# Performance work log

Measured on AMD Instinct MI355X. Metric: run time of the kernel, lower is better.

Reference implementation:

```python
import jax, jax.numpy as jnp
import numpy as np

N_GROUPS = 1024   # n
L = 128           # keys per group
R = 4             # queries per group (nq[i] == R)
NQ_TOTAL = N_GROUPS * R
D_Q = 256
D_K = 256
D_Z = 256
D_V = 256


def setup_inputs() -> dict:
    key = jax.random.key(0)
    ks = jax.random.split(key, 8)
    nq = jnp.full((N_GROUPS,), R, dtype=jnp.int32)
    q = jax.random.normal(ks[0], (NQ_TOTAL, D_Q), dtype=jnp.float32)
    k = jax.random.normal(ks[1], (N_GROUPS, L, D_K), dtype=jnp.float32)
    v = jax.random.normal(ks[2], (N_GROUPS, L, D_V), dtype=jnp.float32)
    m = jax.random.uniform(ks[3], (N_GROUPS, L)) < 0.9
    m = m.at[:, 0].set(True)  # guarantee each row has at least one valid key
    Wq = jax.random.normal(ks[4], (D_Q, D_Z), dtype=jnp.float32) / np.sqrt(D_Q)
    bq = jnp.zeros((D_Z,), dtype=jnp.float32)
    Wk = jax.random.normal(ks[5], (D_K, D_Z), dtype=jnp.float32) / np.sqrt(D_K)
    bk = jnp.zeros((D_Z,), dtype=jnp.float32)
    return {"nq": nq, "q": q, "k": k, "v": v, "m": m,
            "Wq": Wq, "bq": bq, "Wk": Wk, "bk": bk}


def reference(nq, q, v, k, m, Wq, bq, Wk, bk):
    # Linear projections (nn.Linear with bias)
    qz = q @ Wq + bq                      # (N, d_z)
    kz = k @ Wk + bk                      # (n, l, d_z)
    d_z = Wq.shape[1]
    n = m.shape[0]
    # group index per query: equivalent to repeat_interleave(nq, 0)
    gidx = jnp.repeat(jnp.arange(n), nq, total_repeat_length=q.shape[0])  # (N,)
    # scores: s[i, l] = <kz[group(i), l], qz[i]> / sqrt(d_z)
    s = jnp.einsum('ild,id->il', kz[gidx], qz) / jnp.sqrt(jnp.asarray(d_z, qz.dtype))
    s = jnp.where(m[gidx], s, -jnp.inf)   # masked_fill(~m, -inf)
    p = jax.nn.softmax(s, axis=-1)        # softmax over key dim l
    # weighted sum over keys: (N, d)
    return jnp.einsum('il,ild->id', p, v[gidx])
```

## Files before the change

### kernel.cpp

```cpp
#include <hip/hip_runtime.h>

#define D 256
#define LKEYS 128
#define NGROUP 1024
#define NQ 4096

#define MMAT_OFF 0
#define RVEC_OFF (D * D)
#define U_OFF    (RVEC_OFF + D)
#define WS_FLOATS (U_OFF + NQ * D)

#define DOT4(a, b) ((a).x*(b).x + (a).y*(b).y + (a).z*(b).z + (a).w*(b).w)

__global__ __launch_bounds__(256) void prep_kernel(
    const float* __restrict__ Wq, const float* __restrict__ Wk,
    const float* __restrict__ bq, float* __restrict__ Mmat,
    float* __restrict__ rvec)
{
    __shared__ float wq_s[32][65];
    __shared__ float wk_s[32][65];
    __shared__ float bq_s[64];
    const int t  = threadIdx.x;
    const int a0 = (int)(blockIdx.x >> 3) * 32;
    const int b0 = (int)(blockIdx.x & 7) * 32;
    const int ai = t >> 4;
    const int bj = t & 15;
    float acc00 = 0.f, acc01 = 0.f, acc10 = 0.f, acc11 = 0.f;
    float racc = 0.f;
    for (int z0 = 0; z0 < D; z0 += 64) {
        __syncthreads();
        #pragma unroll
        for (int i = 0; i < 2; ++i) {
            const int f4i = t + 256 * i;
            const int row = f4i >> 4;
            const int c   = (f4i & 15) * 4;
            float4 aa = *(const float4*)&Wq[(size_t)(a0 + row) * D + z0 + c];
            wq_s[row][c] = aa.x; wq_s[row][c+1] = aa.y; wq_s[row][c+2] = aa.z; wq_s[row][c+3] = aa.w;
            float4 bb = *(const float4*)&Wk[(size_t)(b0 + row) * D + z0 + c];
            wk_s[row][c] = bb.x; wk_s[row][c+1] = bb.y; wk_s[row][c+2] = bb.z; wk_s[row][c+3] = bb.w;
        }
        if (t < 64) bq_s[t] = bq[z0 + t];
        __syncthreads();
        #pragma unroll 8
        for (int z = 0; z < 64; ++z) {
            const float wq0 = wq_s[ai][z];
            const float wq1 = wq_s[ai + 16][z];
            const float wk0 = wk_s[bj][z];
            const float wk1 = wk_s[bj + 16][z];
            acc00 += wq0 * wk0; acc01 += wq0 * wk1;
            acc10 += wq1 * wk0; acc11 += wq1 * wk1;
        }
        if (a0 == 0 && t < 32) {
            #pragma unroll 8
            for (int z = 0; z < 64; ++z) racc += bq_s[z] * wk_s[t][z];
        }
    }
    Mmat[(size_t)(a0 + ai)      * D + b0 + bj]      = acc00;
    Mmat[(size_t)(a0 + ai)      * D + b0 + bj + 16] = acc01;
    Mmat[(size_t)(a0 + ai + 16) * D + b0 + bj]      = acc10;
    Mmat[(size_t)(a0 + ai + 16) * D + b0 + bj + 16] = acc11;
    if (a0 == 0 && t < 32) rvec[b0 + t] = racc;
}

__global__ __launch_bounds__(256) void u_gemm_kernel(
    const float* __restrict__ q, const float* __restrict__ Mmat,
    const float* __restrict__ rvec, float* __restrict__ uout)
{
    __shared__ float q_s[16][D];
    const int b = blockIdx.x, t = threadIdx.x, lane = t & 63, w = t >> 6;
    {
        const float4* qg = (const float4*)(q + (size_t)b * 16 * D);
        float4* qs4 = (float4*)q_s;
        #pragma unroll
        for (int i = 0; i < 4; ++i) qs4[t + 256 * i] = qg[t + 256 * i];
    }
    __syncthreads();

    const float4* M4 = (const float4*)Mmat;
    const int r0 = w * 4;
    float4 a0 = {0,0,0,0}, a1 = {0,0,0,0}, a2 = {0,0,0,0}, a3 = {0,0,0,0};
    #pragma unroll 4
    for (int kk = 0; kk < D; ++kk) {
        const float4 m4 = M4[kk * 64 + lane];
        const float qa = q_s[r0 + 0][kk], qb = q_s[r0 + 1][kk];
        const float qc = q_s[r0 + 2][kk], qd = q_s[r0 + 3][kk];
        a0.x += qa*m4.x; a0.y += qa*m4.y; a0.z += qa*m4.z; a0.w += qa*m4.w;
        a1.x += qb*m4.x; a1.y += qb*m4.y; a1.z += qb*m4.z; a1.w += qb*m4.w;
        a2.x += qc*m4.x; a2.y += qc*m4.y; a2.z += qc*m4.z; a2.w += qc*m4.w;
        a3.x += qd*m4.x; a3.y += qd*m4.y; a3.z += qd*m4.z; a3.w += qd*m4.w;
    }
    const float4 r4 = ((const float4*)rvec)[lane];
    float4* U4 = (float4*)uout;
    float4 o;
    o.x=(a0.x+r4.x)*0.0625f; o.y=(a0.y+r4.y)*0.0625f; o.z=(a0.z+r4.z)*0.0625f; o.w=(a0.w+r4.w)*0.0625f;
    U4[((size_t)b * 16 + r0 + 0) * 64 + lane] = o;
    o.x=(a1.x+r4.x)*0.0625f; o.y=(a1.y+r4.y)*0.0625f; o.z=(a1.z+r4.z)*0.0625f; o.w=(a1.w+r4.w)*0.0625f;
    U4[((size_t)b * 16 + r0 + 1) * 64 + lane] = o;
    o.x=(a2.x+r4.x)*0.0625f; o.y=(a2.y+r4.y)*0.0625f; o.z=(a2.z+r4.z)*0.0625f; o.w=(a2.w+r4.w)*0.0625f;
    U4[((size_t)b * 16 + r0 + 2) * 64 + lane] = o;
    o.x=(a3.x+r4.x)*0.0625f; o.y=(a3.y+r4.y)*0.0625f; o.z=(a3.z+r4.z)*0.0625f; o.w=(a3.w+r4.w)*0.0625f;
    U4[((size_t)b * 16 + r0 + 3) * 64 + lane] = o;
}

__global__ __launch_bounds__(256, 4) void attn4_kernel(
    const float* __restrict__ k, const float* __restrict__ v,
    const int* __restrict__ m, const float* __restrict__ uws,
    float* __restrict__ out)
{
    const int g = blockIdx.x, t = threadIdx.x, lane = t & 63, w = t >> 6;

    __shared__ float4 part_s[4][4][64];
    __shared__ float  p_t[LKEYS][4];

    const float4* U4 = (const float4*)(uws + (size_t)g * 4 * D);
    const float4 u0 = U4[0 * 64 + lane];
    const float4 u1 = U4[1 * 64 + lane];
    const float4 u2 = U4[2 * 64 + lane];
    const float4 u3 = U4[3 * 64 + lane];

    const int mk = (lane < 32) ? m[(size_t)g * LKEYS + w * 32 + lane] : 0;
    const unsigned long long bal = __ballot(mk != 0);

    const float4* kg = (const float4*)(k + ((size_t)g * LKEYS + w * 32) * D);
    const float4* vg = (const float4*)(v + ((size_t)g * LKEYS + w * 32) * D);

    #pragma unroll
    for (int it = 0; it < 8; ++it) {
        const int kb = it * 4;
        const float4 ka0 = kg[(kb + 0) * 64 + lane];
        const float4 ka1 = kg[(kb + 1) * 64 + lane];
        const float4 ka2 = kg[(kb + 2) * 64 + lane];
        const float4 ka3 = kg[(kb + 3) * 64 + lane];

        float v16[16];
        v16[ 0]=DOT4(ka0,u0); v16[ 1]=DOT4(ka0,u1); v16[ 2]=DOT4(ka0,u2); v16[ 3]=DOT4(ka0,u3);
        v16[ 4]=DOT4(ka1,u0); v16[ 5]=DOT4(ka1,u1); v16[ 6]=DOT4(ka1,u2); v16[ 7]=DOT4(ka1,u3);
        v16[ 8]=DOT4(ka2,u0); v16[ 9]=DOT4(ka2,u1); v16[10]=DOT4(ka2,u2); v16[11]=DOT4(ka2,u3);
        v16[12]=DOT4(ka3,u0); v16[13]=DOT4(ka3,u1); v16[14]=DOT4(ka3,u2); v16[15]=DOT4(ka3,u3);

        float v8[8];
        { const int hb = lane & 1;
          #pragma unroll
          for (int i = 0; i < 8; ++i) {
              const float keep = hb ? v16[8 + i] : v16[i];
              const float send = hb ? v16[i]     : v16[8 + i];
              v8[i] = keep + __shfl_xor(send, 1);
          } }
        float v4a[4];
        { const int hb = (lane >> 1) & 1;
          #pragma unroll
          for (int i = 0; i < 4; ++i) {
              const float keep = hb ? v8[4 + i] : v8[i];
              const float send = hb ? v8[i]     : v8[4 + i];
              v4a[i] = keep + __shfl_xor(send, 2);
          } }
        float v2a[2];
        { const int hb = (lane >> 2) & 1;
          #pragma unroll
          for (int i = 0; i < 2; ++i) {
              const float keep = hb ? v4a[2 + i] : v4a[i];
              const float send = hb ? v4a[i]     : v4a[2 + i];
              v2a[i] = keep + __shfl_xor(send, 4);
          } }
        float v1;
        { const int hb = (lane >> 3) & 1;
          const float keep = hb ? v2a[1] : v2a[0];
          const float send = hb ? v2a[0] : v2a[1];
          v1 = keep + __shfl_xor(send, 8); }
        v1 += __shfl_xor(v1, 16);
        v1 += __shfl_xor(v1, 32);

        if (lane < 16) {
            const int i  = ((lane & 1) << 3) | ((lane & 2) << 1) | ((lane & 4) >> 1) | ((lane & 8) >> 3);
            const int kl = kb + (i >> 2);
            p_t[w * 32 + kl][i & 3] = ((bal >> kl) & 1ull) ? v1 : -1e30f;
        }
    }
    __syncthreads();

    {
        const float s0 = p_t[lane][w];
        const float s1 = p_t[lane + 64][w];
        float mx = fmaxf(s0, s1);
        #pragma unroll
        for (int off = 32; off > 0; off >>= 1) mx = fmaxf(mx, __shfl_xor(mx, off));
        const float e0 = __expf(s0 - mx);
        const float e1 = __expf(s1 - mx);
        float su = e0 + e1;
        #pragma unroll
        for (int off = 32; off > 0; off >>= 1) su += __shfl_xor(su, off);
        const float inv = 1.0f / su;
        p_t[lane][w]      = e0 * inv;
        p_t[lane + 64][w] = e1 * inv;
    }
    __syncthreads();

    float4 a0 = {0,0,0,0}, a1 = {0,0,0,0}, a2 = {0,0,0,0}, a3 = {0,0,0,0};
    #pragma unroll
    for (int it = 0; it < 4; ++it) {
        const int base = it * 8;
        float4 va[8];
        #pragma unroll
        for (int j = 0; j < 8; ++j) va[j] = vg[(base + j) * 64 + lane];
        #pragma unroll
        for (int j = 0; j < 8; ++j) {
            const float4 pr = *(const float4*)&p_t[w * 32 + base + j][0];
            const float4 vv = va[j];
            a0.x += pr.x*vv.x; a0.y += pr.x*vv.y; a0.z += pr.x*vv.z; a0.w += pr.x*vv.w;
            a1.x += pr.y*vv.x; a1.y += pr.y*vv.y; a1.z += pr.y*vv.z; a1.w += pr.y*vv.w;
            a2.x += pr.z*vv.x; a2.y += pr.z*vv.y; a2.z += pr.z*vv.z; a2.w += pr.z*vv.w;
            a3.x += pr.w*vv.x; a3.y += pr.w*vv.y; a3.z += pr.w*vv.z; a3.w += pr.w*vv.w;
        }
    }

    part_s[w][0][lane] = a0; part_s[w][1][lane] = a1;
    part_s[w][2][lane] = a2; part_s[w][3][lane] = a3;
    __syncthreads();
    {
        const float4 r0 = part_s[0][w][lane];
        const float4 r1 = part_s[1][w][lane];
        const float4 r2 = part_s[2][w][lane];
        const float4 r3 = part_s[3][w][lane];
        float4 o;
        o.x = r0.x + r1.x + r2.x + r3.x;
        o.y = r0.y + r1.y + r2.y + r3.y;
        o.z = r0.z + r1.z + r2.z + r3.z;
        o.w = r0.w + r1.w + r2.w + r3.w;
        ((float4*)(out + ((size_t)g * 4 + w) * D))[lane] = o;
    }
}

__global__ __launch_bounds__(256) void attn_kernel(
    const float* __restrict__ q, const float* __restrict__ k,
    const float* __restrict__ v, const int* __restrict__ m,
    const float* __restrict__ Mmat, const float* __restrict__ rvec,
    float* __restrict__ out)
{
    const int g    = blockIdx.x;
    const int t    = threadIdx.x;
    const int lane = t & 63;
    const int w    = t >> 6;

    __shared__ float  q_s[4][D];
    __shared__ float4 part_s[4][4][64];
    __shared__ float4 u_s4[4][64];
    __shared__ float  p_s[4][LKEYS];
    __shared__ int    m_s[LKEYS];

    {
        const float4* qg = (const float4*)(q + (size_t)g * 4 * D);
        ((float4*)q_s)[t] = qg[t];
    }
    if (t < LKEYS) m_s[t] = m[(size_t)g * LKEYS + t];
    __syncthreads();
    {
        const float4* M4 = (const float4*)Mmat;
        float4 p0 = {0,0,0,0}, p1 = {0,0,0,0}, p2 = {0,0,0,0}, p3 = {0,0,0,0};
        const int base = w * 64;
        #pragma unroll 4
        for (int dd = 0; dd < 64; ++dd) {
            const int a = base + dd;
            const float4 m4 = M4[a * 64 + lane];
            const float q0 = q_s[0][a], q1 = q_s[1][a], q2 = q_s[2][a], q3 = q_s[3][a];
            p0.x += q0*m4.x; p0.y += q0*m4.y; p0.z += q0*m4.z; p0.w += q0*m4.w;
            p1.x += q1*m4.x; p1.y += q1*m4.y; p1.z += q1*m4.z; p1.w += q1*m4.w;
            p2.x += q2*m4.x; p2.y += q2*m4.y; p2.z += q2*m4.z; p2.w += q2*m4.w;
            p3.x += q3*m4.x; p3.y += q3*m4.y; p3.z += q3*m4.z; p3.w += q3*m4.w;
        }
        part_s[w][0][lane] = p0; part_s[w][1][lane] = p1;
        part_s[w][2][lane] = p2; part_s[w][3][lane] = p3;
    }
    __syncthreads();
    {
        float4 acc = ((const float4*)rvec)[lane];
        const float4 a0 = part_s[0][w][lane], a1 = part_s[1][w][lane];
        const float4 a2 = part_s[2][w][lane], a3 = part_s[3][w][lane];
        acc.x += a0.x + a1.x + a2.x + a3.x;
        acc.y += a0.y + a1.y + a2.y + a3.y;
        acc.z += a0.z + a1.z + a2.z + a3.z;
        acc.w += a0.w + a1.w + a2.w + a3.w;
        u_s4[w][lane] = acc;
    }
    __syncthreads();

    const float4 u0 = u_s4[0][lane], u1 = u_s4[1][lane];
    const float4 u2 = u_s4[2][lane], u3 = u_s4[3][lane];
    {
        const float4* kg = (const float4*)(k + (size_t)g * LKEYS * D);
        auto reduce_qt = [&](float d0, float d1, float d2, float d3) -> float {
            float keepA = (lane & 1) ? d1 : d0;
            float sendA = (lane & 1) ? d0 : d1;
            keepA += __shfl_xor(sendA, 1);
            float keepB = (lane & 1) ? d3 : d2;
            float sendB = (lane & 1) ? d2 : d3;
            keepB += __shfl_xor(sendB, 1);
            float keep = (lane & 2) ? keepB : keepA;
            float send = (lane & 2) ? keepA : keepB;
            keep += __shfl_xor(send, 2);
            keep += __shfl_xor(keep, 4);
            keep += __shfl_xor(keep, 8);
            keep += __shfl_xor(keep, 16);
            keep += __shfl_xor(keep, 32);
            return keep;
        };
        const int l0 = w * 32;
        for (int kk = 0; kk < 32; kk += 4) {
            const int l = l0 + kk;
            const float4 kA = kg[(l + 0) * 64 + lane];
            const float4 kB = kg[(l + 1) * 64 + lane];
            const float4 kC = kg[(l + 2) * 64 + lane];
            const float4 kD = kg[(l + 3) * 64 + lane];
            float dA0 = DOT4(kA,u0), dA1 = DOT4(kA,u1), dA2 = DOT4(kA,u2), dA3 = DOT4(kA,u3);
            float dB0 = DOT4(kB,u0), dB1 = DOT4(kB,u1), dB2 = DOT4(kB,u2), dB3 = DOT4(kB,u3);
            float dC0 = DOT4(kC,u0), dC1 = DOT4(kC,u1), dC2 = DOT4(kC,u2), dC3 = DOT4(kC,u3);
            float dD0 = DOT4(kD,u0), dD1 = DOT4(kD,u1), dD2 = DOT4(kD,u2), dD3 = DOT4(kD,u3);
            const float rA = reduce_qt(dA0, dA1, dA2, dA3);
            const float rB = reduce_qt(dB0, dB1, dB2, dB3);
            const float rC = reduce_qt(dC0, dC1, dC2, dC3);
            const float rD = reduce_qt(dD0, dD1, dD2, dD3);
            if (lane < 4) {
                p_s[lane][l + 0] = m_s[l + 0] ? rA * 0.0625f : -1e30f;
                p_s[lane][l + 1] = m_s[l + 1] ? rB * 0.0625f : -1e30f;
                p_s[lane][l + 2] = m_s[l + 2] ? rC * 0.0625f : -1e30f;
                p_s[lane][l + 3] = m_s[l + 3] ? rD * 0.0625f : -1e30f;
            }
        }
    }
    __syncthreads();
    {
        const float v0 = p_s[w][lane];
        const float v1 = p_s[w][lane + 64];
        float mx = fmaxf(v0, v1);
        #pragma unroll
        for (int off = 32; off > 0; off >>= 1) mx = fmaxf(mx, __shfl_xor(mx, off));
        const float e0 = __expf(v0 - mx);
        const float e1 = __expf(v1 - mx);
        float sm = e0 + e1;
        #pragma unroll
        for (int off = 32; off > 0; off >>= 1) sm += __shfl_xor(sm, off);
        const float inv = 1.0f / sm;
        p_s[w][lane]      = e0 * inv;
        p_s[w][lane + 64] = e1 * inv;
    }
    {
        const float4* vg = (const float4*)(v + (size_t)g * LKEYS * D);
        float4 acc = {0,0,0,0};
        #pragma unroll 8
        for (int l = 0; l < LKEYS; ++l) {
            const float pw = p_s[w][l];
            const float4 vv = vg[l * 64 + lane];
            acc.x += pw * vv.x; acc.y += pw * vv.y;
            acc.z += pw * vv.z; acc.w += pw * vv.w;
        }
        float4* og = (float4*)(out + ((size_t)g * 4 + w) * D);
        og[lane] = acc;
    }
}

extern "C" void kernel_launch(void* const* d_in, const int* in_sizes, int n_in,
                              void* d_out, int out_size, void* d_ws, size_t ws_size,
                              hipStream_t stream) {
    const float* q  = (const float*)d_in[1];
    const float* k  = (const float*)d_in[2];
    const float* v  = (const float*)d_in[3];
    const int*   m  = (const int*)  d_in[4];
    const float* Wq = (const float*)d_in[5];
    const float* bq = (const float*)d_in[6];
    const float* Wk = (const float*)d_in[7];

    float* ws = (float*)d_ws;
    prep_kernel<<<64, 256, 0, stream>>>(Wq, Wk, bq, ws + MMAT_OFF, ws + RVEC_OFF);

    if (ws_size >= (size_t)WS_FLOATS * sizeof(float)) {
        u_gemm_kernel<<<NQ / 16, 256, 0, stream>>>(q, ws + MMAT_OFF, ws + RVEC_OFF, ws + U_OFF);
        attn4_kernel<<<NGROUP, 256, 0, stream>>>(k, v, m, ws + U_OFF, (float*)d_out);
    } else {
        attn_kernel<<<NGROUP, 256, 0, stream>>>(q, k, v, m, ws + MMAT_OFF, ws + RVEC_OFF,
                                                (float*)d_out);
    }
}
```

Measured before the change: 83.70 us.

## Split each group's keys across two blocks with flash-style softmax combine

The attention kernel now splits each group's 128 keys into two halves, each handled by its own block (2048 blocks). Each block writes unnormalized partial outputs plus its local max and sum to workspace. A new combine kernel merges the two halves with rescaling. The aim is more parallelism and occupancy for the memory-bound key/value streaming. The cost is an extra launch, extra workspace traffic, and a larger workspace requirement, which could send execution to the fallback path if the workspace is too small.

```diff
diff --git a/kernel.cpp b/kernel.cpp
--- a/kernel.cpp
+++ b/kernel.cpp
@@ -8,7 +8,9 @@
 #define MMAT_OFF 0
 #define RVEC_OFF (D * D)
 #define U_OFF    (RVEC_OFF + D)
-#define WS_FLOATS (U_OFF + NQ * D)
+#define PART_OFF (U_OFF + NQ * D)
+#define PART_STRIDE 260
+#define WS_FLOATS (PART_OFF + 2 * NQ * PART_STRIDE)
 
 #define DOT4(a, b) ((a).x*(b).x + (a).y*(b).y + (a).z*(b).z + (a).w*(b).w)
 
@@ -102,15 +104,17 @@
     U4[((size_t)b * 16 + r0 + 3) * 64 + lane] = o;
 }
 
-__global__ __launch_bounds__(256, 4) void attn4_kernel(
+__global__ __launch_bounds__(256, 8) void attn5_kernel(
     const float* __restrict__ k, const float* __restrict__ v,
     const int* __restrict__ m, const float* __restrict__ uws,
-    float* __restrict__ out)
+    float* __restrict__ part)
 {
-    const int g = blockIdx.x, t = threadIdx.x, lane = t & 63, w = t >> 6;
+    const int b = blockIdx.x;
+    const int g = b >> 1, h = b & 1;
+    const int t = threadIdx.x, lane = t & 63, w = t >> 6;
 
     __shared__ float4 part_s[4][4][64];
-    __shared__ float  p_t[LKEYS][4];
+    __shared__ float  p_t[64][4];
 
     const float4* U4 = (const float4*)(uws + (size_t)g * 4 * D);
     const float4 u0 = U4[0 * 64 + lane];
@@ -118,15 +122,16 @@
     const float4 u2 = U4[2 * 64 + lane];
     const float4 u3 = U4[3 * 64 + lane];
 
-    const int mk = (lane < 32) ? m[(size_t)g * LKEYS + w * 32 + lane] : 0;
+    const int kofs = h * 64;
+    const int mk = m[(size_t)g * LKEYS + kofs + lane];
     const unsigned long long bal = __ballot(mk != 0);
 
-    const float4* kg = (const float4*)(k + ((size_t)g * LKEYS + w * 32) * D);
-    const float4* vg = (const float4*)(v + ((size_t)g * LKEYS + w * 32) * D);
+    const float4* kg = (const float4*)(k + ((size_t)g * LKEYS + kofs) * D);
+    const float4* vg = (const float4*)(v + ((size_t)g * LKEYS + kofs) * D);
 
     #pragma unroll
-    for (int it = 0; it < 8; ++it) {
-        const int kb = it * 4;
+    for (int it = 0; it < 4; ++it) {
+        const int kb = w * 16 + it * 4;
         const float4 ka0 = kg[(kb + 0) * 64 + lane];
         const float4 ka1 = kg[(kb + 1) * 64 + lane];
         const float4 ka2 = kg[(kb + 2) * 64 + lane];
@@ -173,38 +178,37 @@
         if (lane < 16) {
             const int i  = ((lane & 1) << 3) | ((lane & 2) << 1) | ((lane & 4) >> 1) | ((lane & 8) >> 3);
             const int kl = kb + (i >> 2);
-            p_t[w * 32 + kl][i & 3] = ((bal >> kl) & 1ull) ? v1 : -1e30f;
-        }
-    }
-    __syncthreads();
-
-    {
-        const float s0 = p_t[lane][w];
-        const float s1 = p_t[lane + 64][w];
-        float mx = fmaxf(s0, s1);
+            p_t[kl][i & 3] = ((bal >> kl) & 1ull) ? v1 : -1e30f;
+        }
+    }
+    __syncthreads();
+
+    float m_loc, su;
+    {
+        const float s = p_t[lane][w];
+        float mx = s;
         #pragma unroll
         for (int off = 32; off > 0; off >>= 1) mx = fmaxf(mx, __shfl_xor(mx, off));
-        const float e0 = __expf(s0 - mx);
-        const float e1 = __expf(s1 - mx);
-        float su = e0 + e1;
-        #pragma unroll
-        for (int off = 32; off > 0; off >>= 1) su += __shfl_xor(su, off);
-        const float inv = 1.0f / su;
-        p_t[lane][w]      = e0 * inv;
-        p_t[lane + 64][w] = e1 * inv;
+        const bool valid = (bal >> lane) & 1ull;
+        const float e = valid ? __expf(s - mx) : 0.f;
+        float ss = e;
+        #pragma unroll
+        for (int off = 32; off > 0; off >>= 1) ss += __shfl_xor(ss, off);
+        p_t[lane][w] = e;
+        m_loc = mx; su = ss;
     }
     __syncthreads();
 
     float4 a0 = {0,0,0,0}, a1 = {0,0,0,0}, a2 = {0,0,0,0}, a3 = {0,0,0,0};
     #pragma unroll
-    for (int it = 0; it < 4; ++it) {
-        const int base = it * 8;
+    for (int it = 0; it < 2; ++it) {
+        const int base = w * 16 + it * 8;
         float4 va[8];
         #pragma unroll
         for (int j = 0; j < 8; ++j) va[j] = vg[(base + j) * 64 + lane];
         #pragma unroll
         for (int j = 0; j < 8; ++j) {
-            const float4 pr = *(const float4*)&p_t[w * 32 + base + j][0];
+            const float4 pr = *(const float4*)&p_t[base + j][0];
             const float4 vv = va[j];
             a0.x += pr.x*vv.x; a0.y += pr.x*vv.y; a0.z += pr.x*vv.z; a0.w += pr.x*vv.w;
             a1.x += pr.y*vv.x; a1.y += pr.y*vv.y; a1.z += pr.y*vv.z; a1.w += pr.y*vv.w;
@@ -226,8 +230,33 @@
         o.y = r0.y + r1.y + r2.y + r3.y;
         o.z = r0.z + r1.z + r2.z + r3.z;
         o.w = r0.w + r1.w + r2.w + r3.w;
-        ((float4*)(out + ((size_t)g * 4 + w) * D))[lane] = o;
-    }
+        float* pb = part + ((size_t)h * NQ + (size_t)g * 4 + w) * PART_STRIDE;
+        ((float4*)pb)[lane] = o;
+        if (lane == 0) { pb[256] = m_loc; pb[257] = su; }
+    }
+}
+
+__global__ __launch_bounds__(256) void combine_kernel(
+    const float* __restrict__ part, float* __restrict__ out)
+{
+    const int b = blockIdx.x, t = threadIdx.x, lane = t & 63, w = t >> 6;
+    const int i = b * 4 + w;
+    const float* pA = part + (size_t)i * PART_STRIDE;
+    const float* pB = part + ((size_t)NQ + i) * PART_STRIDE;
+    const float mA = pA[256], suA = pA[257];
+    const float mB = pB[256], suB = pB[257];
+    const float Mx = fmaxf(mA, mB);
+    const float fA = __expf(mA - Mx);
+    const float fB = __expf(mB - Mx);
+    const float inv = 1.0f / (fA * suA + fB * suB);
+    const float4 aA = ((const float4*)pA)[lane];
+    const float4 aB = ((const float4*)pB)[lane];
+    float4 o;
+    o.x = (fA*aA.x + fB*aB.x) * inv;
+    o.y = (fA*aA.y + fB*aB.y) * inv;
+    o.z = (fA*aA.z + fB*aB.z) * inv;
+    o.w = (fA*aA.w + fB*aB.w) * inv;
+    ((float4*)out)[(size_t)i * 64 + lane] = o;
 }
 
 __global__ __launch_bounds__(256) void attn_kernel(
@@ -373,7 +402,8 @@
 
     if (ws_size >= (size_t)WS_FLOATS * sizeof(float)) {
         u_gemm_kernel<<<NQ / 16, 256, 0, stream>>>(q, ws + MMAT_OFF, ws + RVEC_OFF, ws + U_OFF);
-        attn4_kernel<<<NGROUP, 256, 0, stream>>>(k, v, m, ws + U_OFF, (float*)d_out);
+        attn5_kernel<<<NGROUP * 2, 256, 0, stream>>>(k, v, m, ws + U_OFF, ws + PART_OFF);
+        combine_kernel<<<NGROUP, 256, 0, stream>>>(ws + PART_OFF, (float*)d_out);
     } else {
         attn_kernel<<<NGROUP, 256, 0, stream>>>(q, k, v, m, ws + MMAT_OFF, ws + RVEC_OFF,
                                                 (float*)d_out);
```

New measurement: 104.0 us. 24.3% more time.

## Fuse query-projection GEMM into attention kernel, drop separate u_gemm launch

Applied to the files above, without the earlier changes.

Each attention block now projects its own four queries through Mmat (loading q into shared memory, partial sums per wave, shared-memory reduction) before the score/softmax/value stages, instead of calling a separate u_gemm kernel that wrote U to workspace. This removes one kernel launch and the write and reread of the 4 MB U buffer. In exchange every block streams the full 256 KB Mmat (mostly served from cache), adds two extra block barriers, and drops the occupancy hint of 4 blocks per unit from launch_bounds.

```diff
diff --git a/kernel.cpp b/kernel.cpp
--- a/kernel.cpp
+++ b/kernel.cpp
@@ -3,12 +3,10 @@
 #define D 256
 #define LKEYS 128
 #define NGROUP 1024
-#define NQ 4096
 
 #define MMAT_OFF 0
 #define RVEC_OFF (D * D)
-#define U_OFF    (RVEC_OFF + D)
-#define WS_FLOATS (U_OFF + NQ * D)
+#define WS_FLOATS (RVEC_OFF + D)
 
 #define DOT4(a, b) ((a).x*(b).x + (a).y*(b).y + (a).z*(b).z + (a).w*(b).w)
 
@@ -62,64 +60,63 @@
     if (a0 == 0 && t < 32) rvec[b0 + t] = racc;
 }
 
-__global__ __launch_bounds__(256) void u_gemm_kernel(
-    const float* __restrict__ q, const float* __restrict__ Mmat,
-    const float* __restrict__ rvec, float* __restrict__ uout)
-{
-    __shared__ float q_s[16][D];
-    const int b = blockIdx.x, t = threadIdx.x, lane = t & 63, w = t >> 6;
-    {
-        const float4* qg = (const float4*)(q + (size_t)b * 16 * D);
-        float4* qs4 = (float4*)q_s;
-        #pragma unroll
-        for (int i = 0; i < 4; ++i) qs4[t + 256 * i] = qg[t + 256 * i];
-    }
-    __syncthreads();
-
-    const float4* M4 = (const float4*)Mmat;
-    const int r0 = w * 4;
-    float4 a0 = {0,0,0,0}, a1 = {0,0,0,0}, a2 = {0,0,0,0}, a3 = {0,0,0,0};
-    #pragma unroll 4
-    for (int kk = 0; kk < D; ++kk) {
-        const float4 m4 = M4[kk * 64 + lane];
-        const float qa = q_s[r0 + 0][kk], qb = q_s[r0 + 1][kk];
-        const float qc = q_s[r0 + 2][kk], qd = q_s[r0 + 3][kk];
-        a0.x += qa*m4.x; a0.y += qa*m4.y; a0.z += qa*m4.z; a0.w += qa*m4.w;
-        a1.x += qb*m4.x; a1.y += qb*m4.y; a1.z += qb*m4.z; a1.w += qb*m4.w;
-        a2.x += qc*m4.x; a2.y += qc*m4.y; a2.z += qc*m4.z; a2.w += qc*m4.w;
-        a3.x += qd*m4.x; a3.y += qd*m4.y; a3.z += qd*m4.z; a3.w += qd*m4.w;
-    }
-    const float4 r4 = ((const float4*)rvec)[lane];
-    float4* U4 = (float4*)uout;
-    float4 o;
-    o.x=(a0.x+r4.x)*0.0625f; o.y=(a0.y+r4.y)*0.0625f; o.z=(a0.z+r4.z)*0.0625f; o.w=(a0.w+r4.w)*0.0625f;
-    U4[((size_t)b * 16 + r0 + 0) * 64 + lane] = o;
-    o.x=(a1.x+r4.x)*0.0625f; o.y=(a1.y+r4.y)*0.0625f; o.z=(a1.z+r4.z)*0.0625f; o.w=(a1.w+r4.w)*0.0625f;
-    U4[((size_t)b * 16 + r0 + 1) * 64 + lane] = o;
-    o.x=(a2.x+r4.x)*0.0625f; o.y=(a2.y+r4.y)*0.0625f; o.z=(a2.z+r4.z)*0.0625f; o.w=(a2.w+r4.w)*0.0625f;
-    U4[((size_t)b * 16 + r0 + 2) * 64 + lane] = o;
-    o.x=(a3.x+r4.x)*0.0625f; o.y=(a3.y+r4.y)*0.0625f; o.z=(a3.z+r4.z)*0.0625f; o.w=(a3.w+r4.w)*0.0625f;
-    U4[((size_t)b * 16 + r0 + 3) * 64 + lane] = o;
-}
-
-__global__ __launch_bounds__(256, 4) void attn4_kernel(
-    const float* __restrict__ k, const float* __restrict__ v,
-    const int* __restrict__ m, const float* __restrict__ uws,
+__global__ __launch_bounds__(256) void attn6_kernel(
+    const float* __restrict__ q, const float* __restrict__ k,
+    const float* __restrict__ v, const int* __restrict__ m,
+    const float* __restrict__ Mmat, const float* __restrict__ rvec,
     float* __restrict__ out)
 {
-    const int g = blockIdx.x, t = threadIdx.x, lane = t & 63, w = t >> 6;
-
+    const int g    = blockIdx.x;
+    const int t    = threadIdx.x;
+    const int lane = t & 63;
+    const int w    = t >> 6;
+
+    __shared__ float  q_s[4][D];
     __shared__ float4 part_s[4][4][64];
+    __shared__ float4 u_s4[4][64];
     __shared__ float  p_t[LKEYS][4];
 
-    const float4* U4 = (const float4*)(uws + (size_t)g * 4 * D);
-    const float4 u0 = U4[0 * 64 + lane];
-    const float4 u1 = U4[1 * 64 + lane];
-    const float4 u2 = U4[2 * 64 + lane];
-    const float4 u3 = U4[3 * 64 + lane];
-
+    {
+        const float4* qg = (const float4*)(q + (size_t)g * 4 * D);
+        ((float4*)q_s)[t] = qg[t];
+    }
     const int mk = (lane < 32) ? m[(size_t)g * LKEYS + w * 32 + lane] : 0;
     const unsigned long long bal = __ballot(mk != 0);
+    __syncthreads();
+
+    {
+        const float4* M4 = (const float4*)Mmat;
+        float4 p0 = {0,0,0,0}, p1 = {0,0,0,0}, p2 = {0,0,0,0}, p3 = {0,0,0,0};
+        const int base = w * 64;
+        #pragma unroll 4
+        for (int dd = 0; dd < 64; ++dd) {
+            const int a = base + dd;
+            const float4 m4 = M4[a * 64 + lane];
+            const float q0 = q_s[0][a], q1 = q_s[1][a], q2 = q_s[2][a], q3 = q_s[3][a];
+            p0.x += q0*m4.x; p0.y += q0*m4.y; p0.z += q0*m4.z; p0.w += q0*m4.w;
+            p1.x += q1*m4.x; p1.y += q1*m4.y; p1.z += q1*m4.z; p1.w += q1*m4.w;
+            p2.x += q2*m4.x; p2.y += q2*m4.y; p2.z += q2*m4.z; p2.w += q2*m4.w;
+            p3.x += q3*m4.x; p3.y += q3*m4.y; p3.z += q3*m4.z; p3.w += q3*m4.w;
+        }
+        part_s[w][0][lane] = p0; part_s[w][1][lane] = p1;
+        part_s[w][2][lane] = p2; part_s[w][3][lane] = p3;
+    }
+    __syncthreads();
+
+    {
+        float4 acc = ((const float4*)rvec)[lane];
+        const float4 a0 = part_s[0][w][lane], a1 = part_s[1][w][lane];
+        const float4 a2 = part_s[2][w][lane], a3 = part_s[3][w][lane];
+        acc.x = (acc.x + a0.x + a1.x + a2.x + a3.x) * 0.0625f;
+        acc.y = (acc.y + a0.y + a1.y + a2.y + a3.y) * 0.0625f;
+        acc.z = (acc.z + a0.z + a1.z + a2.z + a3.z) * 0.0625f;
+        acc.w = (acc.w + a0.w + a1.w + a2.w + a3.w) * 0.0625f;
+        u_s4[w][lane] = acc;
+    }
+    __syncthreads();
+
+    const float4 u0 = u_s4[0][lane], u1 = u_s4[1][lane];
+    const float4 u2 = u_s4[2][lane], u3 = u_s4[3][lane];
 
     const float4* kg = (const float4*)(k + ((size_t)g * LKEYS + w * 32) * D);
     const float4* vg = (const float4*)(v + ((size_t)g * LKEYS + w * 32) * D);
@@ -230,133 +227,6 @@
     }
 }
 
-__global__ __launch_bounds__(256) void attn_kernel(
-    const float* __restrict__ q, const float* __restrict__ k,
-    const float* __restrict__ v, const int* __restrict__ m,
-    const float* __restrict__ Mmat, const float* __restrict__ rvec,
-    float* __restrict__ out)
-{
-    const int g    = blockIdx.x;
-    const int t    = threadIdx.x;
-    const int lane = t & 63;
-    const int w    = t >> 6;
-
-    __shared__ float  q_s[4][D];
-    __shared__ float4 part_s[4][4][64];
-    __shared__ float4 u_s4[4][64];
-    __shared__ float  p_s[4][LKEYS];
-    __shared__ int    m_s[LKEYS];
-
-    {
-        const float4* qg = (const float4*)(q + (size_t)g * 4 * D);
-        ((float4*)q_s)[t] = qg[t];
-    }
-    if (t < LKEYS) m_s[t] = m[(size_t)g * LKEYS + t];
-    __syncthreads();
-    {
-        const float4* M4 = (const float4*)Mmat;
-        float4 p0 = {0,0,0,0}, p1 = {0,0,0,0}, p2 = {0,0,0,0}, p3 = {0,0,0,0};
-        const int base = w * 64;
-        #pragma unroll 4
-        for (int dd = 0; dd < 64; ++dd) {
-            const int a = base + dd;
-            const float4 m4 = M4[a * 64 + lane];
-            const float q0 = q_s[0][a], q1 = q_s[1][a], q2 = q_s[2][a], q3 = q_s[3][a];
-            p0.x += q0*m4.x; p0.y += q0*m4.y; p0.z += q0*m4.z; p0.w += q0*m4.w;
-            p1.x += q1*m4.x; p1.y += q1*m4.y; p1.z += q1*m4.z; p1.w += q1*m4.w;
-            p2.x += q2*m4.x; p2.y += q2*m4.y; p2.z += q2*m4.z; p2.w += q2*m4.w;
-            p3.x += q3*m4.x; p3.y += q3*m4.y; p3.z += q3*m4.z; p3.w += q3*m4.w;
-        }
-        part_s[w][0][lane] = p0; part_s[w][1][lane] = p1;
-        part_s[w][2][lane] = p2; part_s[w][3][lane] = p3;
-    }
-    __syncthreads();
-    {
-        float4 acc = ((const float4*)rvec)[lane];
-        const float4 a0 = part_s[0][w][lane], a1 = part_s[1][w][lane];
-        const float4 a2 = part_s[2][w][lane], a3 = part_s[3][w][lane];
-        acc.x += a0.x + a1.x + a2.x + a3.x;
-        acc.y += a0.y + a1.y + a2.y + a3.y;
-        acc.z += a0.z + a1.z + a2.z + a3.z;
-        acc.w += a0.w + a1.w + a2.w + a3.w;
-        u_s4[w][lane] = acc;
-    }
-    __syncthreads();
-
-    const float4 u0 = u_s4[0][lane], u1 = u_s4[1][lane];
-    const float4 u2 = u_s4[2][lane], u3 = u_s4[3][lane];
-    {
-        const float4* kg = (const float4*)(k + (size_t)g * LKEYS * D);
-        auto reduce_qt = [&](float d0, float d1, float d2, float d3) -> float {
-            float keepA = (lane & 1) ? d1 : d0;
-            float sendA = (lane & 1) ? d0 : d1;
-            keepA += __shfl_xor(sendA, 1);
-            float keepB = (lane & 1) ? d3 : d2;
-            float sendB = (lane & 1) ? d2 : d3;
-            keepB += __shfl_xor(sendB, 1);
-            float keep = (lane & 2) ? keepB : keepA;
-            float send = (lane & 2) ? keepA : keepB;
-            keep += __shfl_xor(send, 2);
-            keep += __shfl_xor(keep, 4);
-            keep += __shfl_xor(keep, 8);
-            keep += __shfl_xor(keep, 16);
-            keep += __shfl_xor(keep, 32);
-            return keep;
-        };
-        const int l0 = w * 32;
-        for (int kk = 0; kk < 32; kk += 4) {
-            const int l = l0 + kk;
-            const float4 kA = kg[(l + 0) * 64 + lane];
-            const float4 kB = kg[(l + 1) * 64 + lane];
-            const float4 kC = kg[(l + 2) * 64 + lane];
-            const float4 kD = kg[(l + 3) * 64 + lane];
-            float dA0 = DOT4(kA,u0), dA1 = DOT4(kA,u1), dA2 = DOT4(kA,u2), dA3 = DOT4(kA,u3);
-            float dB0 = DOT4(kB,u0), dB1 = DOT4(kB,u1), dB2 = DOT4(kB,u2), dB3 = DOT4(kB,u3);
-            float dC0 = DOT4(kC,u0), dC1 = DOT4(kC,u1), dC2 = DOT4(kC,u2), dC3 = DOT4(kC,u3);
-            float dD0 = DOT4(kD,u0), dD1 = DOT4(kD,u1), dD2 = DOT4(kD,u2), dD3 = DOT4(kD,u3);
-            const float rA = reduce_qt(dA0, dA1, dA2, dA3);
-            const float rB = reduce_qt(dB0, dB1, dB2, dB3);
-            const float rC = reduce_qt(dC0, dC1, dC2, dC3);
-            const float rD = reduce_qt(dD0, dD1, dD2, dD3);
-            if (lane < 4) {
-                p_s[lane][l + 0] = m_s[l + 0] ? rA * 0.0625f : -1e30f;
-                p_s[lane][l + 1] = m_s[l + 1] ? rB * 0.0625f : -1e30f;
-                p_s[lane][l + 2] = m_s[l + 2] ? rC * 0.0625f : -1e30f;
-                p_s[lane][l + 3] = m_s[l + 3] ? rD * 0.0625f : -1e30f;
-            }
-        }
-    }
-    __syncthreads();
-    {
-        const float v0 = p_s[w][lane];
-        const float v1 = p_s[w][lane + 64];
-        float mx = fmaxf(v0, v1);
-        #pragma unroll
-        for (int off = 32; off > 0; off >>= 1) mx = fmaxf(mx, __shfl_xor(mx, off));
-        const float e0 = __expf(v0 - mx);
-        const float e1 = __expf(v1 - mx);
-        float sm = e0 + e1;
-        #pragma unroll
-        for (int off = 32; off > 0; off >>= 1) sm += __shfl_xor(sm, off);
-        const float inv = 1.0f / sm;
-        p_s[w][lane]      = e0 * inv;
-        p_s[w][lane + 64] = e1 * inv;
-    }
-    {
-        const float4* vg = (const float4*)(v + (size_t)g * LKEYS * D);
-        float4 acc = {0,0,0,0};
-        #pragma unroll 8
-        for (int l = 0; l < LKEYS; ++l) {
-            const float pw = p_s[w][l];
-            const float4 vv = vg[l * 64 + lane];
-            acc.x += pw * vv.x; acc.y += pw * vv.y;
-            acc.z += pw * vv.z; acc.w += pw * vv.w;
-        }
-        float4* og = (float4*)(out + ((size_t)g * 4 + w) * D);
-        og[lane] = acc;
-    }
-}
-
 extern "C" void kernel_launch(void* const* d_in, const int* in_sizes, int n_in,
                               void* d_out, int out_size, void* d_ws, size_t ws_size,
                               hipStream_t stream) {
@@ -370,12 +240,6 @@
 
     float* ws = (float*)d_ws;
     prep_kernel<<<64, 256, 0, stream>>>(Wq, Wk, bq, ws + MMAT_OFF, ws + RVEC_OFF);
-
-    if (ws_size >= (size_t)WS_FLOATS * sizeof(float)) {
-        u_gemm_kernel<<<NQ / 16, 256, 0, stream>>>(q, ws + MMAT_OFF, ws + RVEC_OFF, ws + U_OFF);
-        attn4_kernel<<<NGROUP, 256, 0, stream>>>(k, v, m, ws + U_OFF, (float*)d_out);
-    } else {
-        attn_kernel<<<NGROUP, 256, 0, stream>>>(q, k, v, m, ws + MMAT_OFF, ws + RVEC_OFF,
-                                                (float*)d_out);
-    }
+    attn6_kernel<<<NGROUP, 256, 0, stream>>>(q, k, v, m, ws + MMAT_OFF, ws + RVEC_OFF,
+                                             (float*)d_out);
 }
```

Measured after the change: 69.46 us. -17.0%, faster.
